# Kernel optimization log

Hardware: AMD Instinct MI355X
Metric: run time of the kernel (lower is better)

Reference implementation:

```python
import jax, jax.numpy as jnp
import numpy as np

K = 3          # kernel size (implied by 18/27 offset channels)
PAD = 1
STRIDE = 1


def setup_inputs() -> dict:
    key = jax.random.key(0)
    k0, k1, k2 = jax.random.split(key, 3)
    B, C, H, W = 4, 256, 64, 64
    Cout = 256
    x = jax.random.normal(k0, (B, C, H, W), jnp.float32)
    # offset/mask predicting conv: 18 offset + 9 mask channels (deform_group=1)
    w_off = jax.random.normal(k1, (27, C, K, K), jnp.float32) * 0.01
    b_off = jnp.zeros((27,), jnp.float32)
    # main deformable conv weight (bias=False)
    w = jax.random.normal(k2, (Cout, C, K, K), jnp.float32) * 0.05
    return {"x": x, "w_off": w_off, "b_off": b_off, "w": w}


def _modulated_dcn(x, w_off, b_off, w):
    B, C, H, W = x.shape
    KK = K * K
    # regular conv predicting offsets (+ mask)
    om = jax.lax.conv_general_dilated(
        x, w_off, (STRIDE, STRIDE), [(PAD, PAD), (PAD, PAD)],
        dimension_numbers=("NCHW", "OIHW", "NCHW")) + b_off[None, :, None, None]
    Ho, Wo = om.shape[2], om.shape[3]
    # channel layout: interleaved (dy, dx) per kernel tap, then 9 mask channels
    off = om[:, :2 * KK].reshape(B, KK, 2, Ho, Wo)
    mask = jax.nn.sigmoid(om[:, 2 * KK:3 * KK])            # (B, KK, Ho, Wo)

    ky, kx = jnp.meshgrid(jnp.arange(K), jnp.arange(K), indexing="ij")
    base_y = (jnp.arange(Ho) * STRIDE - PAD)[:, None]       # (Ho, 1)
    base_x = (jnp.arange(Wo) * STRIDE - PAD)[None, :]       # (1, Wo)
    # sampling positions p = p0 + pn + offset, shape (B, KK, Ho, Wo)
    py = base_y[None, None] + ky.reshape(KK)[None, :, None, None] + off[:, :, 0]
    px = base_x[None, None] + kx.reshape(KK)[None, :, None, None] + off[:, :, 1]

    y0f = jnp.floor(py)
    x0f = jnp.floor(px)
    ly = py - y0f
    lx = px - x0f
    y0 = y0f.astype(jnp.int32)
    x0 = x0f.astype(jnp.int32)

    xf = x.reshape(B, C, H * W)

    def samp(yi, xi):
        valid = ((yi >= 0) & (yi < H) & (xi >= 0) & (xi < W)).astype(x.dtype)
        idx = jnp.clip(yi, 0, H - 1) * W + jnp.clip(xi, 0, W - 1)
        v = jnp.take_along_axis(xf, idx.reshape(B, 1, -1), axis=2)
        return v.reshape(B, C, KK, Ho, Wo) * valid[:, None]

    # bilinear interpolation with zero padding outside the image
    v = (samp(y0,     x0    ) * ((1 - ly) * (1 - lx))[:, None]
         + samp(y0,     x0 + 1) * ((1 - ly) * lx)[:, None]
         + samp(y0 + 1, x0    ) * (ly * (1 - lx))[:, None]
         + samp(y0 + 1, x0 + 1) * (ly * lx)[:, None])
    v = v * mask[:, None]                                   # modulation
    # conv as contraction over (Cin, KK)
    return jnp.einsum("bckhw,ock->bohw", v, w.reshape(w.shape[0], C, KK))


def reference(x, w_off, b_off, w):
    return _modulated_dcn(x, w_off, b_off, w)
```

## Files before the change

kernel.cpp:

```cpp
#include <hip/hip_runtime.h>
#include <math.h>

#define HH 64
#define WW 64
#define CIN 256
#define COUT 256
#define KKT 9
#define HWSZ 4096
#define VP 260

typedef __bf16  v8bf   __attribute__((ext_vector_type(8)));
typedef float   v4f    __attribute__((ext_vector_type(4)));
typedef short   short8 __attribute__((ext_vector_type(8)));
typedef unsigned short ushort4v __attribute__((ext_vector_type(4)));

__device__ inline unsigned short f2bf(float f) {
    union { float f; unsigned u; } uf; uf.f = f;
    unsigned r = uf.u + 0x7fff + ((uf.u >> 16) & 1);
    return (unsigned short)(r >> 16);
}
__device__ inline float bf2f(unsigned short u) {
    union { unsigned u; float f; } uf; uf.u = ((unsigned)u) << 16;
    return uf.f;
}

__global__ __launch_bounds__(256) void k_prep(const float* __restrict__ x,
                                              const float* __restrict__ w,
                                              const float* __restrict__ w_off,
                                              unsigned short* __restrict__ x_t,
                                              unsigned short* __restrict__ wprep,
                                              unsigned short* __restrict__ woffp) {
    __shared__ float s_w[2304];
    int id  = blockIdx.x;
    int tid = threadIdx.x;
    if (id < 256) {
        int b  = id >> 6;
        int h  = id & 63;
        int px  = tid & 63;
        int oct = tid >> 6;
        const float* xr = x + (((size_t)b * CIN) * HH + h) * WW;
        unsigned short* orow = x_t + (((size_t)id) * WW + px) * CIN;
        for (int g = 0; g < 8; g++) {
            int cb = g * 32 + oct * 8;
            unsigned short v[8];
#pragma unroll
            for (int j = 0; j < 8; j++)
                v[j] = f2bf(xr[(size_t)(cb + j) * HWSZ + px]);
            *(short8*)(orow + cb) = *(short8*)v;
        }
    } else if (id < 512) {
        int o = id - 256;
        for (int i = tid; i < 2304; i += 256) s_w[i] = w[(size_t)o * 2304 + i];
        __syncthreads();
        for (int u = tid; u < 576; u += 256) {
            int t  = u >> 3;
            int kq = u & 7;
            unsigned short v[4];
#pragma unroll
            for (int j = 0; j < 4; j++) {
                int kp = t * 32 + kq * 4 + j;
                int kk = kp >> 8;
                int c  = kp & 255;
                v[j] = f2bf(s_w[c * 9 + kk]);
            }
            *(ushort4v*)&wprep[((size_t)(t * 256 + o)) * 32 + kq * 4] = *(ushort4v*)v;
        }
    } else {
        int t = id - 512;
#pragma unroll
        for (int i = 0; i < 4; i++) {
            int idx = i * 256 + tid;
            int och = idx >> 5;
            int ki  = idx & 31;
            int kp  = t * 32 + ki;
            int kk  = kp >> 8;
            int c   = kp & 255;
            float v = (och < 27) ? w_off[((size_t)och * 256 + c) * 9 + kk] : 0.f;
            woffp[(size_t)t * 1024 + idx] = f2bf(v);
        }
    }
}

__global__ __launch_bounds__(256) void k_off_mfma(const unsigned short* __restrict__ x_t,
                                                  const unsigned short* __restrict__ woffp,
                                                  const float* __restrict__ b_off,
                                                  float* __restrict__ om) {
    int id    = blockIdx.x;
    int g     = id & 7;
    int phalf = (id >> 3) & 1;
    int hi    = (id >> 4) & 7;
    int b     = id >> 7;
    int h     = g * 8 + hi;
    int p0    = phalf * 32;
    int tid  = threadIdx.x;
    int lane = tid & 63;
    int wv   = tid >> 6;
    int g2   = wv >> 1;
    int ntw  = wv & 1;
    int m16  = lane & 15;
    int quad = lane >> 4;

    __shared__ unsigned short s_row[3 * 34 * VP];
    __shared__ float s_red[2][32][33];

    const unsigned short* xb = x_t + (size_t)b * HWSZ * CIN;

    for (int u = tid; u < 3 * 1088; u += 256) {
        int row = u / 1088;
        int rem = u - row * 1088;
        int px  = rem >> 5;
        int c8  = (rem & 31) * 8;
        int y   = h + row - 1;
        int xg  = p0 + px - 1;
        short8 val = (short8)0;
        if ((unsigned)y < HH && (unsigned)xg < WW)
            val = *(const short8*)(xb + ((size_t)y * WW + xg) * CIN + c8);
        *(short8*)&s_row[(row * 34 + px) * VP + c8] = val;
    }
    __syncthreads();

    v4f acc[2];
    acc[0] = (v4f)(0.f);
    acc[1] = (v4f)(0.f);

#pragma unroll
    for (int ky = 0; ky < 3; ky++) {
#pragma unroll
        for (int kx = 0; kx < 3; kx++) {
#pragma unroll
            for (int c2 = 0; c2 < 4; c2++) {
                int ch = c2 * 2 + g2;
                int t  = (ky * 3 + kx) * 8 + ch;
                const unsigned short* wp = woffp + (size_t)t * 1024;
                short8 af0 = *(const short8*)(wp + m16 * 32 + quad * 8);
                short8 af1 = *(const short8*)(wp + (16 + m16) * 32 + quad * 8);
                short8 bfr = *(const short8*)
                    &s_row[(ky * 34 + ntw * 16 + m16 + kx) * VP + ch * 32 + quad * 8];
                acc[0] = __builtin_amdgcn_mfma_f32_16x16x32_bf16(
                    __builtin_bit_cast(v8bf, af0), __builtin_bit_cast(v8bf, bfr), acc[0], 0, 0, 0);
                acc[1] = __builtin_amdgcn_mfma_f32_16x16x32_bf16(
                    __builtin_bit_cast(v8bf, af1), __builtin_bit_cast(v8bf, bfr), acc[1], 0, 0, 0);
            }
        }
    }

#pragma unroll
    for (int mt = 0; mt < 2; mt++)
#pragma unroll
        for (int r = 0; r < 4; r++)
            s_red[g2][mt * 16 + quad * 4 + r][ntw * 16 + m16] = acc[mt][r];
    __syncthreads();

    for (int i2 = tid; i2 < 27 * 32; i2 += 256) {
        int och = i2 >> 5;
        int px  = i2 & 31;
        float s = s_red[0][och][px] + s_red[1][och][px] + b_off[och];
        om[((size_t)b * 27 + och) * HWSZ + h * WW + p0 + px] = s;
    }
}

__global__ __launch_bounds__(512, 4) void k_main(const unsigned short* __restrict__ x_t,
                                                 const float* __restrict__ om,
                                                 const unsigned short* __restrict__ wprep,
                                                 float* __restrict__ out) {
    int id    = blockIdx.x;
    int g     = id & 7;
    int phalf = (id >> 3) & 1;
    int hi    = (id >> 4) & 7;
    int b     = id >> 7;
    int h     = g * 8 + hi;
    int p0    = phalf * 32;
    int tid  = threadIdx.x;
    int lane = tid & 63;
    int oct  = tid >> 6;
    int m16  = lane & 15;
    int quad = lane >> 4;

    __shared__ int4   s_base[KKT][32];
    __shared__ float4 s_wt  [KKT][32];
    __shared__ unsigned short s_v[32 * VP];

    const float* omb = om + (size_t)b * 27 * HWSZ + h * WW;
    for (int i = tid; i < KKT * 32; i += 512) {
        int kk = i >> 5;
        int pl = i & 31;
        int p  = p0 + pl;
        float offy = omb[(size_t)(2 * kk)     * HWSZ + p];
        float offx = omb[(size_t)(2 * kk + 1) * HWSZ + p];
        float mv   = omb[(size_t)(18 + kk)    * HWSZ + p];
        int ky = kk / 3, kx = kk - 3 * (kk / 3);
        float py = (float)(h - 1 + ky) + offy;
        float px = (float)(p - 1 + kx) + offx;
        float y0f = floorf(py);
        float x0f = floorf(px);
        float ly = py - y0f, lx = px - x0f;
        int y0 = (int)y0f, x0 = (int)x0f;
        float m = 1.f / (1.f + __expf(-mv));
        bool yv0 = (unsigned)y0       < HH;
        bool yv1 = (unsigned)(y0 + 1) < HH;
        bool xv0 = (unsigned)x0       < WW;
        bool xv1 = (unsigned)(x0 + 1) < WW;
        int y0c = min(max(y0, 0), HH - 1);
        int y1c = min(max(y0 + 1, 0), HH - 1);
        int x0c = min(max(x0, 0), WW - 1);
        int x1c = min(max(x0 + 1, 0), WW - 1);
        s_base[kk][pl] = make_int4((y0c * WW + x0c) * CIN, (y0c * WW + x1c) * CIN,
                                   (y1c * WW + x0c) * CIN, (y1c * WW + x1c) * CIN);
        s_wt[kk][pl] = make_float4(
            (yv0 && xv0) ? (1.f - ly) * (1.f - lx) * m : 0.f,
            (yv0 && xv1) ? (1.f - ly) * lx         * m : 0.f,
            (yv1 && xv0) ? ly * (1.f - lx)         * m : 0.f,
            (yv1 && xv1) ? ly * lx                 * m : 0.f);
    }
    __syncthreads();

    v4f acc[2][2];
#pragma unroll
    for (int mt = 0; mt < 2; mt++)
#pragma unroll
        for (int nt = 0; nt < 2; nt++) acc[mt][nt] = (v4f)(0.f);

    const unsigned short* xb = x_t + (size_t)b * HWSZ * CIN;
    const unsigned short* xc = xb + lane * 4;

    for (int kk = 0; kk < KKT; kk++) {
#pragma unroll
        for (int i = 0; i < 4; i++) {
            int pl = oct * 4 + i;
            int4   bp = s_base[kk][pl];
            float4 wt = s_wt[kk][pl];
            ushort4v t0 = *(const ushort4v*)(xc + bp.x);
            ushort4v t1 = *(const ushort4v*)(xc + bp.y);
            ushort4v t2 = *(const ushort4v*)(xc + bp.z);
            ushort4v t3 = *(const ushort4v*)(xc + bp.w);
            unsigned short vv[4];
#pragma unroll
            for (int j = 0; j < 4; j++) {
                float val = wt.x * bf2f(t0[j]) + wt.y * bf2f(t1[j])
                          + wt.z * bf2f(t2[j]) + wt.w * bf2f(t3[j]);
                vv[j] = f2bf(val);
            }
            *(ushort4v*)&s_v[pl * VP + lane * 4] = *(ushort4v*)vv;
        }
        __syncthreads();

#pragma unroll 2
        for (int ch = 0; ch < 8; ch++) {
            int t = kk * 8 + ch;
            const unsigned short* wp = wprep + ((size_t)t * 256 + oct * 32) * 32;
            short8 af0 = *(const short8*)(wp + m16 * 32 + quad * 8);
            short8 af1 = *(const short8*)(wp + (16 + m16) * 32 + quad * 8);
            short8 bfr[2];
#pragma unroll
            for (int nt = 0; nt < 2; nt++)
                bfr[nt] = *(const short8*)&s_v[(nt * 16 + m16) * VP + ch * 32 + quad * 8];
#pragma unroll
            for (int nt = 0; nt < 2; nt++) {
                acc[0][nt] = __builtin_amdgcn_mfma_f32_16x16x32_bf16(
                    __builtin_bit_cast(v8bf, af0), __builtin_bit_cast(v8bf, bfr[nt]),
                    acc[0][nt], 0, 0, 0);
                acc[1][nt] = __builtin_amdgcn_mfma_f32_16x16x32_bf16(
                    __builtin_bit_cast(v8bf, af1), __builtin_bit_cast(v8bf, bfr[nt]),
                    acc[1][nt], 0, 0, 0);
            }
        }
        __syncthreads();
    }

    float* ob = out + ((size_t)b * COUT) * HWSZ + h * WW + p0;
#pragma unroll
    for (int mt = 0; mt < 2; mt++)
#pragma unroll
        for (int nt = 0; nt < 2; nt++)
#pragma unroll
            for (int r = 0; r < 4; r++) {
                int o = oct * 32 + mt * 16 + quad * 4 + r;
                ob[(size_t)o * HWSZ + nt * 16 + m16] = acc[mt][nt][r];
            }
}

extern "C" void kernel_launch(void* const* d_in, const int* in_sizes, int n_in,
                              void* d_out, int out_size, void* d_ws, size_t ws_size,
                              hipStream_t stream) {
    const float* x     = (const float*)d_in[0];
    const float* w_off = (const float*)d_in[1];
    const float* b_off = (const float*)d_in[2];
    const float* w     = (const float*)d_in[3];
    float* out = (float*)d_out;

    float* om = (float*)d_ws;
    unsigned short* x_t   = (unsigned short*)(om + 442368);
    unsigned short* wprep = x_t + (size_t)4 * HWSZ * CIN;
    unsigned short* woffp = wprep + 589824;

    hipLaunchKernelGGL(k_prep,     dim3(584), dim3(256), 0, stream, x, w, w_off, x_t, wprep, woffp);
    hipLaunchKernelGGL(k_off_mfma, dim3(512), dim3(256), 0, stream, x_t, woffp, b_off, om);
    hipLaunchKernelGGL(k_main,     dim3(512), dim3(512), 0, stream, x_t, om, wprep, out);
}
```

Baseline: 145.5 us.

## Fuse offset conv into main deformable kernel and double-buffer sampled tile

Measured after the change: 169.8 us. 1.17x slower.

```diff
diff --git a/kernel.cpp b/kernel.cpp
--- a/kernel.cpp
+++ b/kernel.cpp
@@ -81,87 +81,10 @@
     }
 }
 
-__global__ __launch_bounds__(256) void k_off_mfma(const unsigned short* __restrict__ x_t,
-                                                  const unsigned short* __restrict__ woffp,
-                                                  const float* __restrict__ b_off,
-                                                  float* __restrict__ om) {
-    int id    = blockIdx.x;
-    int g     = id & 7;
-    int phalf = (id >> 3) & 1;
-    int hi    = (id >> 4) & 7;
-    int b     = id >> 7;
-    int h     = g * 8 + hi;
-    int p0    = phalf * 32;
-    int tid  = threadIdx.x;
-    int lane = tid & 63;
-    int wv   = tid >> 6;
-    int g2   = wv >> 1;
-    int ntw  = wv & 1;
-    int m16  = lane & 15;
-    int quad = lane >> 4;
-
-    __shared__ unsigned short s_row[3 * 34 * VP];
-    __shared__ float s_red[2][32][33];
-
-    const unsigned short* xb = x_t + (size_t)b * HWSZ * CIN;
-
-    for (int u = tid; u < 3 * 1088; u += 256) {
-        int row = u / 1088;
-        int rem = u - row * 1088;
-        int px  = rem >> 5;
-        int c8  = (rem & 31) * 8;
-        int y   = h + row - 1;
-        int xg  = p0 + px - 1;
-        short8 val = (short8)0;
-        if ((unsigned)y < HH && (unsigned)xg < WW)
-            val = *(const short8*)(xb + ((size_t)y * WW + xg) * CIN + c8);
-        *(short8*)&s_row[(row * 34 + px) * VP + c8] = val;
-    }
-    __syncthreads();
-
-    v4f acc[2];
-    acc[0] = (v4f)(0.f);
-    acc[1] = (v4f)(0.f);
-
-#pragma unroll
-    for (int ky = 0; ky < 3; ky++) {
-#pragma unroll
-        for (int kx = 0; kx < 3; kx++) {
-#pragma unroll
-            for (int c2 = 0; c2 < 4; c2++) {
-                int ch = c2 * 2 + g2;
-                int t  = (ky * 3 + kx) * 8 + ch;
-                const unsigned short* wp = woffp + (size_t)t * 1024;
-                short8 af0 = *(const short8*)(wp + m16 * 32 + quad * 8);
-                short8 af1 = *(const short8*)(wp + (16 + m16) * 32 + quad * 8);
-                short8 bfr = *(const short8*)
-                    &s_row[(ky * 34 + ntw * 16 + m16 + kx) * VP + ch * 32 + quad * 8];
-                acc[0] = __builtin_amdgcn_mfma_f32_16x16x32_bf16(
-                    __builtin_bit_cast(v8bf, af0), __builtin_bit_cast(v8bf, bfr), acc[0], 0, 0, 0);
-                acc[1] = __builtin_amdgcn_mfma_f32_16x16x32_bf16(
-                    __builtin_bit_cast(v8bf, af1), __builtin_bit_cast(v8bf, bfr), acc[1], 0, 0, 0);
-            }
-        }
-    }
-
-#pragma unroll
-    for (int mt = 0; mt < 2; mt++)
-#pragma unroll
-        for (int r = 0; r < 4; r++)
-            s_red[g2][mt * 16 + quad * 4 + r][ntw * 16 + m16] = acc[mt][r];
-    __syncthreads();
-
-    for (int i2 = tid; i2 < 27 * 32; i2 += 256) {
-        int och = i2 >> 5;
-        int px  = i2 & 31;
-        float s = s_red[0][och][px] + s_red[1][och][px] + b_off[och];
-        om[((size_t)b * 27 + och) * HWSZ + h * WW + p0 + px] = s;
-    }
-}
-
 __global__ __launch_bounds__(512, 4) void k_main(const unsigned short* __restrict__ x_t,
-                                                 const float* __restrict__ om,
                                                  const unsigned short* __restrict__ wprep,
+                                                 const unsigned short* __restrict__ woffp,
+                                                 const float* __restrict__ b_off,
                                                  float* __restrict__ out) {
     int id    = blockIdx.x;
     int g     = id & 7;
@@ -176,18 +99,59 @@
     int m16  = lane & 15;
     int quad = lane >> 4;
 
+    __shared__ union {
+        unsigned short v[2][32 * VP];
+        float red[4][32][33];
+    } s_u;
     __shared__ int4   s_base[KKT][32];
     __shared__ float4 s_wt  [KKT][32];
-    __shared__ unsigned short s_v[32 * VP];
-
-    const float* omb = om + (size_t)b * 27 * HWSZ + h * WW;
+
+    const unsigned short* xb = x_t + (size_t)b * HWSZ * CIN;
+
+    {
+        int ks  = oct >> 1;
+        int ntw = oct & 1;
+        v4f aco[2];
+        aco[0] = (v4f)(0.f);
+        aco[1] = (v4f)(0.f);
+#pragma unroll 3
+        for (int j = 0; j < 18; j++) {
+            int t  = j * 4 + ks;
+            int kk = t >> 3;
+            int ch = t & 7;
+            int ky = kk / 3 - 1;
+            int kx = kk - 3 * (kk / 3) - 1;
+            const unsigned short* wp = woffp + (size_t)t * 1024;
+            short8 af0 = *(const short8*)(wp + m16 * 32 + quad * 8);
+            short8 af1 = *(const short8*)(wp + (16 + m16) * 32 + quad * 8);
+            int y  = h + ky;
+            int xg = p0 + ntw * 16 + m16 + kx;
+            short8 bfr = (short8)0;
+            if ((unsigned)y < HH && (unsigned)xg < WW)
+                bfr = *(const short8*)(xb + ((size_t)y * WW + xg) * CIN + ch * 32 + quad * 8);
+            aco[0] = __builtin_amdgcn_mfma_f32_16x16x32_bf16(
+                __builtin_bit_cast(v8bf, af0), __builtin_bit_cast(v8bf, bfr), aco[0], 0, 0, 0);
+            aco[1] = __builtin_amdgcn_mfma_f32_16x16x32_bf16(
+                __builtin_bit_cast(v8bf, af1), __builtin_bit_cast(v8bf, bfr), aco[1], 0, 0, 0);
+        }
+#pragma unroll
+        for (int mt = 0; mt < 2; mt++)
+#pragma unroll
+            for (int r = 0; r < 4; r++)
+                s_u.red[ks][mt * 16 + quad * 4 + r][ntw * 16 + m16] = aco[mt][r];
+    }
+    __syncthreads();
+
     for (int i = tid; i < KKT * 32; i += 512) {
         int kk = i >> 5;
         int pl = i & 31;
         int p  = p0 + pl;
-        float offy = omb[(size_t)(2 * kk)     * HWSZ + p];
-        float offx = omb[(size_t)(2 * kk + 1) * HWSZ + p];
-        float mv   = omb[(size_t)(18 + kk)    * HWSZ + p];
+        float offy = s_u.red[0][2 * kk][pl]     + s_u.red[1][2 * kk][pl]
+                   + s_u.red[2][2 * kk][pl]     + s_u.red[3][2 * kk][pl]     + b_off[2 * kk];
+        float offx = s_u.red[0][2 * kk + 1][pl] + s_u.red[1][2 * kk + 1][pl]
+                   + s_u.red[2][2 * kk + 1][pl] + s_u.red[3][2 * kk + 1][pl] + b_off[2 * kk + 1];
+        float mv   = s_u.red[0][18 + kk][pl]    + s_u.red[1][18 + kk][pl]
+                   + s_u.red[2][18 + kk][pl]    + s_u.red[3][18 + kk][pl]    + b_off[18 + kk];
         int ky = kk / 3, kx = kk - 3 * (kk / 3);
         float py = (float)(h - 1 + ky) + offy;
         float px = (float)(p - 1 + kx) + offx;
@@ -220,10 +184,11 @@
 #pragma unroll
         for (int nt = 0; nt < 2; nt++) acc[mt][nt] = (v4f)(0.f);
 
-    const unsigned short* xb = x_t + (size_t)b * HWSZ * CIN;
     const unsigned short* xc = xb + lane * 4;
 
     for (int kk = 0; kk < KKT; kk++) {
+        unsigned short* vbuf = s_u.v[kk & 1];
+
 #pragma unroll
         for (int i = 0; i < 4; i++) {
             int pl = oct * 4 + i;
@@ -240,11 +205,11 @@
                           + wt.z * bf2f(t2[j]) + wt.w * bf2f(t3[j]);
                 vv[j] = f2bf(val);
             }
-            *(ushort4v*)&s_v[pl * VP + lane * 4] = *(ushort4v*)vv;
+            *(ushort4v*)&vbuf[pl * VP + lane * 4] = *(ushort4v*)vv;
         }
         __syncthreads();
 
-#pragma unroll 2
+#pragma unroll
         for (int ch = 0; ch < 8; ch++) {
             int t = kk * 8 + ch;
             const unsigned short* wp = wprep + ((size_t)t * 256 + oct * 32) * 32;
@@ -253,7 +218,7 @@
             short8 bfr[2];
 #pragma unroll
             for (int nt = 0; nt < 2; nt++)
-                bfr[nt] = *(const short8*)&s_v[(nt * 16 + m16) * VP + ch * 32 + quad * 8];
+                bfr[nt] = *(const short8*)&vbuf[(nt * 16 + m16) * VP + ch * 32 + quad * 8];
 #pragma unroll
             for (int nt = 0; nt < 2; nt++) {
                 acc[0][nt] = __builtin_amdgcn_mfma_f32_16x16x32_bf16(
@@ -264,7 +229,6 @@
                     acc[1][nt], 0, 0, 0);
             }
         }
-        __syncthreads();
     }
 
     float* ob = out + ((size_t)b * COUT) * HWSZ + h * WW + p0;
@@ -288,12 +252,10 @@
     const float* w     = (const float*)d_in[3];
     float* out = (float*)d_out;
 
-    float* om = (float*)d_ws;
-    unsigned short* x_t   = (unsigned short*)(om + 442368);
+    unsigned short* x_t   = (unsigned short*)d_ws;
     unsigned short* wprep = x_t + (size_t)4 * HWSZ * CIN;
     unsigned short* woffp = wprep + 589824;
 
-    hipLaunchKernelGGL(k_prep,     dim3(584), dim3(256), 0, stream, x, w, w_off, x_t, wprep, woffp);
-    hipLaunchKernelGGL(k_off_mfma, dim3(512), dim3(256), 0, stream, x_t, woffp, b_off, om);
-    hipLaunchKernelGGL(k_main,     dim3(512), dim3(512), 0, stream, x_t, om, wprep, out);
-}
+    hipLaunchKernelGGL(k_prep, dim3(584), dim3(256), 0, stream, x, w, w_off, x_t, wprep, woffp);
+    hipLaunchKernelGGL(k_main, dim3(512), dim3(512), 0, stream, x_t, wprep, woffp, b_off, out);
+}
```

## Widen main block to full row, double-buffer sampled tile, coalesce prep transpose

Applied to the files above, without the earlier changes.

New measurement: 233.1 us. +60.2%, slower.

```diff
diff --git a/kernel.cpp b/kernel.cpp
--- a/kernel.cpp
+++ b/kernel.cpp
@@ -8,6 +8,7 @@
 #define KKT 9
 #define HWSZ 4096
 #define VP 260
+#define TP 258
 
 typedef __bf16  v8bf   __attribute__((ext_vector_type(8)));
 typedef float   v4f    __attribute__((ext_vector_type(4)));
@@ -30,27 +31,38 @@
                                               unsigned short* __restrict__ x_t,
                                               unsigned short* __restrict__ wprep,
                                               unsigned short* __restrict__ woffp) {
-    __shared__ float s_w[2304];
+    __shared__ union {
+        unsigned short t[64 * TP];
+        float w[2304];
+    } s;
     int id  = blockIdx.x;
     int tid = threadIdx.x;
     if (id < 256) {
-        int b  = id >> 6;
-        int h  = id & 63;
-        int px  = tid & 63;
-        int oct = tid >> 6;
-        const float* xr = x + (((size_t)b * CIN) * HH + h) * WW;
-        unsigned short* orow = x_t + (((size_t)id) * WW + px) * CIN;
-        for (int g = 0; g < 8; g++) {
-            int cb = g * 32 + oct * 8;
-            unsigned short v[8];
-#pragma unroll
-            for (int j = 0; j < 8; j++)
-                v[j] = f2bf(xr[(size_t)(cb + j) * HWSZ + px]);
-            *(short8*)(orow + cb) = *(short8*)v;
+        int b = id >> 6;
+        int h = id & 63;
+#pragma unroll
+        for (int i = 0; i < 16; i++) {
+            int idx = i * 256 + tid;
+            int c   = idx >> 4;
+            int q   = idx & 15;
+            float4 v = *(const float4*)&x[(((size_t)b * CIN + c) * HH + h) * WW + q * 4];
+            s.t[(q * 4 + 0) * TP + c] = f2bf(v.x);
+            s.t[(q * 4 + 1) * TP + c] = f2bf(v.y);
+            s.t[(q * 4 + 2) * TP + c] = f2bf(v.z);
+            s.t[(q * 4 + 3) * TP + c] = f2bf(v.w);
+        }
+        __syncthreads();
+#pragma unroll
+        for (int i = 0; i < 8; i++) {
+            int idx = i * 256 + tid;
+            int px  = idx >> 5;
+            int c8  = idx & 31;
+            *(short8*)&x_t[(((size_t)id) * 64 + px) * CIN + c8 * 8] =
+                *(short8*)&s.t[px * TP + c8 * 8];
         }
     } else if (id < 512) {
         int o = id - 256;
-        for (int i = tid; i < 2304; i += 256) s_w[i] = w[(size_t)o * 2304 + i];
+        for (int i = tid; i < 2304; i += 256) s.w[i] = w[(size_t)o * 2304 + i];
         __syncthreads();
         for (int u = tid; u < 576; u += 256) {
             int t  = u >> 3;
@@ -61,7 +73,7 @@
                 int kp = t * 32 + kq * 4 + j;
                 int kk = kp >> 8;
                 int c  = kp & 255;
-                v[j] = f2bf(s_w[c * 9 + kk]);
+                v[j] = f2bf(s.w[c * 9 + kk]);
             }
             *(ushort4v*)&wprep[((size_t)(t * 256 + o)) * 32 + kq * 4] = *(ushort4v*)v;
         }
@@ -159,32 +171,27 @@
     }
 }
 
-__global__ __launch_bounds__(512, 4) void k_main(const unsigned short* __restrict__ x_t,
-                                                 const float* __restrict__ om,
-                                                 const unsigned short* __restrict__ wprep,
-                                                 float* __restrict__ out) {
-    int id    = blockIdx.x;
-    int g     = id & 7;
-    int phalf = (id >> 3) & 1;
-    int hi    = (id >> 4) & 7;
-    int b     = id >> 7;
-    int h     = g * 8 + hi;
-    int p0    = phalf * 32;
+__global__ __launch_bounds__(1024, 4) void k_main(const unsigned short* __restrict__ x_t,
+                                                  const float* __restrict__ om,
+                                                  const unsigned short* __restrict__ wprep,
+                                                  float* __restrict__ out) {
+    int id = blockIdx.x;
+    int b  = id >> 6;
+    int h  = id & 63;
     int tid  = threadIdx.x;
     int lane = tid & 63;
-    int oct  = tid >> 6;
+    int wv   = tid >> 6;
     int m16  = lane & 15;
     int quad = lane >> 4;
 
-    __shared__ int4   s_base[KKT][32];
-    __shared__ float4 s_wt  [KKT][32];
-    __shared__ unsigned short s_v[32 * VP];
+    __shared__ int4   s_base[KKT][64];
+    __shared__ float4 s_wt  [KKT][64];
+    __shared__ unsigned short s_v[2][64 * VP];
 
     const float* omb = om + (size_t)b * 27 * HWSZ + h * WW;
-    for (int i = tid; i < KKT * 32; i += 512) {
-        int kk = i >> 5;
-        int pl = i & 31;
-        int p  = p0 + pl;
+    for (int i = tid; i < KKT * 64; i += 1024) {
+        int kk = i >> 6;
+        int p  = i & 63;
         float offy = omb[(size_t)(2 * kk)     * HWSZ + p];
         float offx = omb[(size_t)(2 * kk + 1) * HWSZ + p];
         float mv   = omb[(size_t)(18 + kk)    * HWSZ + p];
@@ -204,9 +211,9 @@
         int y1c = min(max(y0 + 1, 0), HH - 1);
         int x0c = min(max(x0, 0), WW - 1);
         int x1c = min(max(x0 + 1, 0), WW - 1);
-        s_base[kk][pl] = make_int4((y0c * WW + x0c) * CIN, (y0c * WW + x1c) * CIN,
-                                   (y1c * WW + x0c) * CIN, (y1c * WW + x1c) * CIN);
-        s_wt[kk][pl] = make_float4(
+        s_base[kk][p] = make_int4((y0c * WW + x0c) * CIN, (y0c * WW + x1c) * CIN,
+                                  (y1c * WW + x0c) * CIN, (y1c * WW + x1c) * CIN);
+        s_wt[kk][p] = make_float4(
             (yv0 && xv0) ? (1.f - ly) * (1.f - lx) * m : 0.f,
             (yv0 && xv1) ? (1.f - ly) * lx         * m : 0.f,
             (yv1 && xv0) ? ly * (1.f - lx)         * m : 0.f,
@@ -214,19 +221,19 @@
     }
     __syncthreads();
 
-    v4f acc[2][2];
-#pragma unroll
-    for (int mt = 0; mt < 2; mt++)
-#pragma unroll
-        for (int nt = 0; nt < 2; nt++) acc[mt][nt] = (v4f)(0.f);
+    v4f acc[4];
+#pragma unroll
+    for (int nt = 0; nt < 4; nt++) acc[nt] = (v4f)(0.f);
 
     const unsigned short* xb = x_t + (size_t)b * HWSZ * CIN;
     const unsigned short* xc = xb + lane * 4;
 
     for (int kk = 0; kk < KKT; kk++) {
+        unsigned short* vbuf = s_v[kk & 1];
+
 #pragma unroll
         for (int i = 0; i < 4; i++) {
-            int pl = oct * 4 + i;
+            int pl = wv * 4 + i;
             int4   bp = s_base[kk][pl];
             float4 wt = s_wt[kk][pl];
             ushort4v t0 = *(const ushort4v*)(xc + bp.x);
@@ -240,43 +247,35 @@
                           + wt.z * bf2f(t2[j]) + wt.w * bf2f(t3[j]);
                 vv[j] = f2bf(val);
             }
-            *(ushort4v*)&s_v[pl * VP + lane * 4] = *(ushort4v*)vv;
+            *(ushort4v*)&vbuf[pl * VP + lane * 4] = *(ushort4v*)vv;
         }
         __syncthreads();
 
-#pragma unroll 2
+#pragma unroll
         for (int ch = 0; ch < 8; ch++) {
             int t = kk * 8 + ch;
-            const unsigned short* wp = wprep + ((size_t)t * 256 + oct * 32) * 32;
-            short8 af0 = *(const short8*)(wp + m16 * 32 + quad * 8);
-            short8 af1 = *(const short8*)(wp + (16 + m16) * 32 + quad * 8);
-            short8 bfr[2];
-#pragma unroll
-            for (int nt = 0; nt < 2; nt++)
-                bfr[nt] = *(const short8*)&s_v[(nt * 16 + m16) * VP + ch * 32 + quad * 8];
-#pragma unroll
-            for (int nt = 0; nt < 2; nt++) {
-                acc[0][nt] = __builtin_amdgcn_mfma_f32_16x16x32_bf16(
-                    __builtin_bit_cast(v8bf, af0), __builtin_bit_cast(v8bf, bfr[nt]),
-                    acc[0][nt], 0, 0, 0);
-                acc[1][nt] = __builtin_amdgcn_mfma_f32_16x16x32_bf16(
-                    __builtin_bit_cast(v8bf, af1), __builtin_bit_cast(v8bf, bfr[nt]),
-                    acc[1][nt], 0, 0, 0);
-            }
-        }
-        __syncthreads();
-    }
-
-    float* ob = out + ((size_t)b * COUT) * HWSZ + h * WW + p0;
-#pragma unroll
-    for (int mt = 0; mt < 2; mt++)
-#pragma unroll
-        for (int nt = 0; nt < 2; nt++)
-#pragma unroll
-            for (int r = 0; r < 4; r++) {
-                int o = oct * 32 + mt * 16 + quad * 4 + r;
-                ob[(size_t)o * HWSZ + nt * 16 + m16] = acc[mt][nt][r];
-            }
+            const unsigned short* wp = wprep + ((size_t)t * 256 + wv * 16) * 32;
+            short8 af = *(const short8*)(wp + m16 * 32 + quad * 8);
+            short8 bfr[4];
+#pragma unroll
+            for (int nt = 0; nt < 4; nt++)
+                bfr[nt] = *(const short8*)&vbuf[(nt * 16 + m16) * VP + ch * 32 + quad * 8];
+#pragma unroll
+            for (int nt = 0; nt < 4; nt++)
+                acc[nt] = __builtin_amdgcn_mfma_f32_16x16x32_bf16(
+                    __builtin_bit_cast(v8bf, af), __builtin_bit_cast(v8bf, bfr[nt]),
+                    acc[nt], 0, 0, 0);
+        }
+    }
+
+    float* ob = out + ((size_t)b * COUT) * HWSZ + h * WW;
+#pragma unroll
+    for (int nt = 0; nt < 4; nt++)
+#pragma unroll
+        for (int r = 0; r < 4; r++) {
+            int o = wv * 16 + quad * 4 + r;
+            ob[(size_t)o * HWSZ + nt * 16 + m16] = acc[nt][r];
+        }
 }
 
 extern "C" void kernel_launch(void* const* d_in, const int* in_sizes, int n_in,
@@ -293,7 +292,7 @@
     unsigned short* wprep = x_t + (size_t)4 * HWSZ * CIN;
     unsigned short* woffp = wprep + 589824;
 
-    hipLaunchKernelGGL(k_prep,     dim3(584), dim3(256), 0, stream, x, w, w_off, x_t, wprep, woffp);
-    hipLaunchKernelGGL(k_off_mfma, dim3(512), dim3(256), 0, stream, x_t, woffp, b_off, om);
-    hipLaunchKernelGGL(k_main,     dim3(512), dim3(512), 0, stream, x_t, om, wprep, out);
-}
+    hipLaunchKernelGGL(k_prep,     dim3(584), dim3(256),  0, stream, x, w, w_off, x_t, wprep, woffp);
+    hipLaunchKernelGGL(k_off_mfma, dim3(512), dim3(256),  0, stream, x_t, woffp, b_off, om);
+    hipLaunchKernelGGL(k_main,     dim3(256), dim3(1024), 0, stream, x_t, om, wprep, out);
+}
```

## Transpose x via LDS in prep and double-buffer sampled tile in deform conv

Applied to the files above, without the earlier changes.

Result: slower. 172.4 us (+18.5%).

```diff
diff --git a/kernel.cpp b/kernel.cpp
--- a/kernel.cpp
+++ b/kernel.cpp
@@ -8,6 +8,7 @@
 #define KKT 9
 #define HWSZ 4096
 #define VP 260
+#define TP 258
 
 typedef __bf16  v8bf   __attribute__((ext_vector_type(8)));
 typedef float   v4f    __attribute__((ext_vector_type(4)));
@@ -30,27 +31,38 @@
                                               unsigned short* __restrict__ x_t,
                                               unsigned short* __restrict__ wprep,
                                               unsigned short* __restrict__ woffp) {
-    __shared__ float s_w[2304];
+    __shared__ union {
+        unsigned short t[64 * TP];
+        float w[2304];
+    } s;
     int id  = blockIdx.x;
     int tid = threadIdx.x;
     if (id < 256) {
-        int b  = id >> 6;
-        int h  = id & 63;
-        int px  = tid & 63;
-        int oct = tid >> 6;
-        const float* xr = x + (((size_t)b * CIN) * HH + h) * WW;
-        unsigned short* orow = x_t + (((size_t)id) * WW + px) * CIN;
-        for (int g = 0; g < 8; g++) {
-            int cb = g * 32 + oct * 8;
-            unsigned short v[8];
-#pragma unroll
-            for (int j = 0; j < 8; j++)
-                v[j] = f2bf(xr[(size_t)(cb + j) * HWSZ + px]);
-            *(short8*)(orow + cb) = *(short8*)v;
+        int b = id >> 6;
+        int h = id & 63;
+#pragma unroll
+        for (int i = 0; i < 16; i++) {
+            int idx = i * 256 + tid;
+            int c   = idx >> 4;
+            int q   = idx & 15;
+            float4 v = *(const float4*)&x[(((size_t)b * CIN + c) * HH + h) * WW + q * 4];
+            s.t[(q * 4 + 0) * TP + c] = f2bf(v.x);
+            s.t[(q * 4 + 1) * TP + c] = f2bf(v.y);
+            s.t[(q * 4 + 2) * TP + c] = f2bf(v.z);
+            s.t[(q * 4 + 3) * TP + c] = f2bf(v.w);
+        }
+        __syncthreads();
+#pragma unroll
+        for (int i = 0; i < 8; i++) {
+            int idx = i * 256 + tid;
+            int px  = idx >> 5;
+            int c8  = idx & 31;
+            *(short8*)&x_t[(((size_t)id) * 64 + px) * CIN + c8 * 8] =
+                *(short8*)&s.t[px * TP + c8 * 8];
         }
     } else if (id < 512) {
         int o = id - 256;
-        for (int i = tid; i < 2304; i += 256) s_w[i] = w[(size_t)o * 2304 + i];
+        for (int i = tid; i < 2304; i += 256) s.w[i] = w[(size_t)o * 2304 + i];
         __syncthreads();
         for (int u = tid; u < 576; u += 256) {
             int t  = u >> 3;
@@ -61,7 +73,7 @@
                 int kp = t * 32 + kq * 4 + j;
                 int kk = kp >> 8;
                 int c  = kp & 255;
-                v[j] = f2bf(s_w[c * 9 + kk]);
+                v[j] = f2bf(s.w[c * 9 + kk]);
             }
             *(ushort4v*)&wprep[((size_t)(t * 256 + o)) * 32 + kq * 4] = *(ushort4v*)v;
         }
@@ -178,7 +190,7 @@
 
     __shared__ int4   s_base[KKT][32];
     __shared__ float4 s_wt  [KKT][32];
-    __shared__ unsigned short s_v[32 * VP];
+    __shared__ unsigned short s_v[2][32 * VP];
 
     const float* omb = om + (size_t)b * 27 * HWSZ + h * WW;
     for (int i = tid; i < KKT * 32; i += 512) {
@@ -224,6 +236,8 @@
     const unsigned short* xc = xb + lane * 4;
 
     for (int kk = 0; kk < KKT; kk++) {
+        unsigned short* vbuf = s_v[kk & 1];
+
 #pragma unroll
         for (int i = 0; i < 4; i++) {
             int pl = oct * 4 + i;
@@ -240,7 +254,7 @@
                           + wt.z * bf2f(t2[j]) + wt.w * bf2f(t3[j]);
                 vv[j] = f2bf(val);
             }
-            *(ushort4v*)&s_v[pl * VP + lane * 4] = *(ushort4v*)vv;
+            *(ushort4v*)&vbuf[pl * VP + lane * 4] = *(ushort4v*)vv;
         }
         __syncthreads();
 
@@ -253,7 +267,7 @@
             short8 bfr[2];
 #pragma unroll
             for (int nt = 0; nt < 2; nt++)
-                bfr[nt] = *(const short8*)&s_v[(nt * 16 + m16) * VP + ch * 32 + quad * 8];
+                bfr[nt] = *(const short8*)&vbuf[(nt * 16 + m16) * VP + ch * 32 + quad * 8];
 #pragma unroll
             for (int nt = 0; nt < 2; nt++) {
                 acc[0][nt] = __builtin_amdgcn_mfma_f32_16x16x32_bf16(
@@ -264,7 +278,6 @@
                     acc[1][nt], 0, 0, 0);
             }
         }
-        __syncthreads();
     }
 
     float* ob = out + ((size_t)b * COUT) * HWSZ + h * WW + p0;
```
